# Optimization experiments

Measured on AMD Instinct MI355X. Metric: run time of the kernel, lower is better.

Reference implementation:

```python
import jax, jax.numpy as jnp
import numpy as np

B, T, C = 4, 2048, 384
NUM_HEADS, HEAD_SIZE = 6, 64


def setup_inputs() -> dict:
    key = jax.random.key(0)
    ks = jax.random.split(key, 6)
    s = 1.0 / np.sqrt(C)
    return {
        "x": jax.random.normal(ks[0], (B, T, C), dtype=jnp.float32),
        "Wq": jax.random.normal(ks[1], (C, NUM_HEADS * HEAD_SIZE), dtype=jnp.float32) * s,
        "bq": jnp.zeros((NUM_HEADS * HEAD_SIZE,), dtype=jnp.float32),
        "Wk": jax.random.normal(ks[2], (C, NUM_HEADS * HEAD_SIZE), dtype=jnp.float32) * s,
        "bk": jnp.zeros((NUM_HEADS * HEAD_SIZE,), dtype=jnp.float32),
        "Wv": jax.random.normal(ks[3], (C, NUM_HEADS * HEAD_SIZE), dtype=jnp.float32) * s,
        "bv": jnp.zeros((NUM_HEADS * HEAD_SIZE,), dtype=jnp.float32),
        "Wo": jax.random.normal(ks[4], (NUM_HEADS * HEAD_SIZE, C), dtype=jnp.float32) * s,
        "bo": jnp.zeros((C,), dtype=jnp.float32),
    }


def reference(x, Wq, bq, Wk, bk, Wv, bv, Wo, bo):
    b, t, c = x.shape
    h, d = NUM_HEADS, HEAD_SIZE
    q = (x @ Wq + bq).reshape(b, t, h, d)
    k = (x @ Wk + bk).reshape(b, t, h, d)
    v = (x @ Wv + bv).reshape(b, t, h, d)
    scores = jnp.einsum('bthd,bshd->bhts', q, k) / jnp.sqrt(jnp.float32(d))
    causal = jnp.tril(jnp.ones((t, t), dtype=bool))  # [t,t]
    scores = jnp.where(causal, scores, -jnp.inf)
    weights = jax.nn.softmax(scores, axis=-1)  # dropout identity (inference)
    ctx = jnp.einsum('bhts,bshd->bthd', weights, v).reshape(b, t, h * d)
    return ctx @ Wo + bo
```

## Files before the change

### kernel.cpp

```cpp
#include <hip/hip_runtime.h>

#define B_  4
#define T_  2048
#define C_  384
#define NH_ 6
#define HS_ 64
#define M_  (B_*T_)

typedef float floatx4 __attribute__((ext_vector_type(4)));
typedef __bf16 bf16x8 __attribute__((ext_vector_type(8)));
typedef unsigned short ushort_t;
typedef unsigned short ushortx8 __attribute__((ext_vector_type(8)));
typedef unsigned short ushortx4 __attribute__((ext_vector_type(4)));

__device__ __forceinline__ ushort_t f2bf(float f) {
    unsigned u = __builtin_bit_cast(unsigned, f);
    unsigned r = (u + 0x7FFFu + ((u >> 16) & 1u)) >> 16;
    return (ushort_t)r;
}

__global__ __launch_bounds__(256) void prep(
    const float* __restrict__ x, ushort_t* __restrict__ xb,
    const float* __restrict__ Wq, const float* __restrict__ Wk,
    const float* __restrict__ Wv, const float* __restrict__ Wo,
    ushort_t* __restrict__ Wtq, ushort_t* __restrict__ Wtk,
    ushort_t* __restrict__ Wtv, ushort_t* __restrict__ Wto)
{
    __shared__ float Ls[64][65];
    const int tid = threadIdx.x;
    const int bx = blockIdx.x;

    if (bx < 1536) {
        const int i = (bx * 256 + tid) * 8;
        const float4 a = *(const float4*)&x[i];
        const float4 b = *(const float4*)&x[i + 4];
        ushortx8 p;
        p[0] = f2bf(a.x); p[1] = f2bf(a.y); p[2] = f2bf(a.z); p[3] = f2bf(a.w);
        p[4] = f2bf(b.x); p[5] = f2bf(b.y); p[6] = f2bf(b.z); p[7] = f2bf(b.w);
        *(ushortx8*)&xb[i] = p;
        return;
    }

    const int idx = bx - 1536;
    const int z = idx / 36, rest = idx % 36;
    const float* __restrict__ W = (z == 0) ? Wq : (z == 1) ? Wk : (z == 2) ? Wv : Wo;
    ushort_t* __restrict__ Wt   = (z == 0) ? Wtq : (z == 1) ? Wtk : (z == 2) ? Wtv : Wto;
    const int k0 = (rest / 6) * 64, n0 = (rest % 6) * 64;

    #pragma unroll
    for (int p = 0; p < 4; ++p) {
        const int kk = p * 16 + (tid >> 4);
        const int nn = (tid & 15) * 4;
        const float4 v = *(const float4*)&W[(size_t)(k0 + kk) * 384 + n0 + nn];
        Ls[kk][nn] = v.x; Ls[kk][nn + 1] = v.y; Ls[kk][nn + 2] = v.z; Ls[kk][nn + 3] = v.w;
    }
    __syncthreads();
    #pragma unroll
    for (int p = 0; p < 4; ++p) {
        const int n = p * 16 + (tid >> 4);
        const int kc = (tid & 15) * 4;
        ushortx4 pk;
        #pragma unroll
        for (int t = 0; t < 4; ++t) pk[t] = f2bf(Ls[kc + t][n]);
        *(ushortx4*)&Wt[(size_t)(n0 + n) * 384 + k0 + kc] = pk;
    }
}

__global__ __launch_bounds__(256) void qkv_gemm(
    const ushort_t* __restrict__ xb,
    const ushort_t* __restrict__ Wtq, const ushort_t* __restrict__ Wtk,
    const ushort_t* __restrict__ Wtv,
    const float* __restrict__ bq, const float* __restrict__ bk, const float* __restrict__ bv,
    ushort_t* __restrict__ Qb, ushort_t* __restrict__ Kb, ushort_t* __restrict__ Vtb)
{
    __shared__ ushort_t Sm[2][8192];

    const int tid  = threadIdx.x;
    const int lane = tid & 63;
    const int wv   = tid >> 6;
    const int m    = lane & 15;
    const int quad = lane >> 4;

    const int t0 = blockIdx.x * 128;
    const int n0 = blockIdx.y * 128;
    const int which = n0 / 384;
    const int n_in0 = n0 % 384;
    const bool isV = (which == 2);

    const ushort_t* __restrict__ Wt = (which == 0) ? Wtq : (which == 1) ? Wtk : Wtv;

    const int aOff = isV ? 0 : 4096;
    const int bOff = isV ? 4096 : 0;
    const int a0 = (wv & 1) * 64;
    const int b0 = (wv >> 1) * 64;

    const int rs0 = tid >> 2,         cs0 = tid & 3;
    const int rs1 = (tid + 256) >> 2, cs1 = tid & 3;
    const int sw0 = ((cs0 ^ ((rs0 >> 1) & 3)) << 3);
    const int sw1 = ((cs1 ^ ((rs1 >> 1) & 3)) << 3);

    floatx4 acc[4][4];
    #pragma unroll
    for (int i = 0; i < 4; ++i)
        #pragma unroll
        for (int j = 0; j < 4; ++j) acc[i][j] = (floatx4){0.f, 0.f, 0.f, 0.f};

    ushortx8 xr0 = *(const ushortx8*)&xb[(size_t)(t0 + rs0) * 384 + cs0 * 8];
    ushortx8 xr1 = *(const ushortx8*)&xb[(size_t)(t0 + rs1) * 384 + cs1 * 8];
    ushortx8 wr0 = *(const ushortx8*)&Wt[(size_t)(n_in0 + rs0) * 384 + cs0 * 8];
    ushortx8 wr1 = *(const ushortx8*)&Wt[(size_t)(n_in0 + rs1) * 384 + cs1 * 8];

    for (int ks = 0; ks < 12; ++ks) {
        ushort_t* __restrict__ S = &Sm[ks & 1][0];
        *(ushortx8*)&S[rs0 * 32 + sw0] = xr0;
        *(ushortx8*)&S[rs1 * 32 + sw1] = xr1;
        *(ushortx8*)&S[4096 + rs0 * 32 + sw0] = wr0;
        *(ushortx8*)&S[4096 + rs1 * 32 + sw1] = wr1;
        __syncthreads();

        if (ks < 11) {
            const int kk = (ks + 1) * 32;
            xr0 = *(const ushortx8*)&xb[(size_t)(t0 + rs0) * 384 + kk + cs0 * 8];
            xr1 = *(const ushortx8*)&xb[(size_t)(t0 + rs1) * 384 + kk + cs1 * 8];
            wr0 = *(const ushortx8*)&Wt[(size_t)(n_in0 + rs0) * 384 + kk + cs0 * 8];
            wr1 = *(const ushortx8*)&Wt[(size_t)(n_in0 + rs1) * 384 + kk + cs1 * 8];
        }

        bf16x8 fA[4], fB[4];
        #pragma unroll
        for (int i = 0; i < 4; ++i) {
            const int ra = a0 + i * 16 + m;
            fA[i] = *(const bf16x8*)&S[aOff + ra * 32 + ((quad ^ ((ra >> 1) & 3)) << 3)];
        }
        #pragma unroll
        for (int j = 0; j < 4; ++j) {
            const int rb = b0 + j * 16 + m;
            fB[j] = *(const bf16x8*)&S[bOff + rb * 32 + ((quad ^ ((rb >> 1) & 3)) << 3)];
        }
        #pragma unroll
        for (int i = 0; i < 4; ++i)
            #pragma unroll
            for (int j = 0; j < 4; ++j)
                acc[i][j] = __builtin_amdgcn_mfma_f32_16x16x32_bf16(fA[i], fB[j], acc[i][j], 0, 0, 0);
    }

    if (!isV) {
        ushort_t* __restrict__ out = (which == 0) ? Qb : Kb;
        const float* __restrict__ bias = (which == 0) ? bq : bk;
        const float scale = (which == 0) ? 0.125f : 1.0f;
        #pragma unroll
        for (int i = 0; i < 4; ++i) {
            const int n_base = n_in0 + a0 + i * 16 + quad * 4;
            const int h = n_base >> 6, d0 = n_base & 63;
            #pragma unroll
            for (int j = 0; j < 4; ++j) {
                const int tg = t0 + b0 + j * 16 + m;
                const int b = tg >> 11, tb = tg & (T_ - 1);
                ushortx4 pk;
                #pragma unroll
                for (int r = 0; r < 4; ++r)
                    pk[r] = f2bf((acc[i][j][r] + bias[n_base + r]) * scale);
                *(ushortx4*)&out[(((size_t)(b * NH_ + h)) * T_ + tb) * HS_ + d0] = pk;
            }
        }
    } else {
        #pragma unroll
        for (int i = 0; i < 4; ++i) {
            const int tg0 = t0 + a0 + i * 16 + quad * 4;
            const int b = tg0 >> 11, tb0 = tg0 & (T_ - 1);
            #pragma unroll
            for (int j = 0; j < 4; ++j) {
                const int n_l = n_in0 + b0 + j * 16 + m;
                const int h = n_l >> 6, d = n_l & 63;
                const float bb = bv[n_l];
                ushortx4 pk;
                #pragma unroll
                for (int r = 0; r < 4; ++r) pk[r] = f2bf(acc[i][j][r] + bb);
                *(ushortx4*)&Vtb[(((size_t)(b * NH_ + h)) * HS_ + d) * T_ + tb0] = pk;
            }
        }
    }
}

__global__ __launch_bounds__(256) void proj_gemm(
    const ushort_t* __restrict__ ctxb,
    const ushort_t* __restrict__ Wto,
    const float* __restrict__ bo,
    float* __restrict__ out)
{
    __shared__ ushort_t Sm[2][6144];

    const int tid  = threadIdx.x;
    const int lane = tid & 63;
    const int wv   = tid >> 6;
    const int m    = lane & 15;
    const int quad = lane >> 4;

    const int t0 = blockIdx.x * 64;
    const int n0 = blockIdx.y * 128;
    const int a0 = (wv & 1) * 64;
    const int b0 = (wv >> 1) * 32;

    const int rc = tid >> 2,          cc = tid & 3;
    const int rw0 = tid >> 2,         cw0 = tid & 3;
    const int rw1 = (tid + 256) >> 2, cw1 = tid & 3;
    const int swc  = ((cc  ^ ((rc  >> 1) & 3)) << 3);
    const int sww0 = ((cw0 ^ ((rw0 >> 1) & 3)) << 3);
    const int sww1 = ((cw1 ^ ((rw1 >> 1) & 3)) << 3);

    floatx4 acc[4][2];
    #pragma unroll
    for (int i = 0; i < 4; ++i)
        #pragma unroll
        for (int j = 0; j < 2; ++j) acc[i][j] = (floatx4){0.f, 0.f, 0.f, 0.f};

    ushortx8 cr  = *(const ushortx8*)&ctxb[(size_t)(t0 + rc) * 384 + cc * 8];
    ushortx8 wr0 = *(const ushortx8*)&Wto[(size_t)(n0 + rw0) * 384 + cw0 * 8];
    ushortx8 wr1 = *(const ushortx8*)&Wto[(size_t)(n0 + rw1) * 384 + cw1 * 8];

    for (int ks = 0; ks < 12; ++ks) {
        ushort_t* __restrict__ S = &Sm[ks & 1][0];
        *(ushortx8*)&S[rc * 32 + swc] = cr;
        *(ushortx8*)&S[2048 + rw0 * 32 + sww0] = wr0;
        *(ushortx8*)&S[2048 + rw1 * 32 + sww1] = wr1;
        __syncthreads();

        if (ks < 11) {
            const int kk = (ks + 1) * 32;
            cr  = *(const ushortx8*)&ctxb[(size_t)(t0 + rc) * 384 + kk + cc * 8];
            wr0 = *(const ushortx8*)&Wto[(size_t)(n0 + rw0) * 384 + kk + cw0 * 8];
            wr1 = *(const ushortx8*)&Wto[(size_t)(n0 + rw1) * 384 + kk + cw1 * 8];
        }

        bf16x8 fA[4], fB[2];
        #pragma unroll
        for (int i = 0; i < 4; ++i) {
            const int ra = a0 + i * 16 + m;
            fA[i] = *(const bf16x8*)&S[2048 + ra * 32 + ((quad ^ ((ra >> 1) & 3)) << 3)];
        }
        #pragma unroll
        for (int j = 0; j < 2; ++j) {
            const int rb = b0 + j * 16 + m;
            fB[j] = *(const bf16x8*)&S[rb * 32 + ((quad ^ ((rb >> 1) & 3)) << 3)];
        }
        #pragma unroll
        for (int i = 0; i < 4; ++i)
            #pragma unroll
            for (int j = 0; j < 2; ++j)
                acc[i][j] = __builtin_amdgcn_mfma_f32_16x16x32_bf16(fA[i], fB[j], acc[i][j], 0, 0, 0);
    }

    #pragma unroll
    for (int i = 0; i < 4; ++i) {
        const int n_base = n0 + a0 + i * 16 + quad * 4;
        const float4 bb = *(const float4*)&bo[n_base];
        #pragma unroll
        for (int j = 0; j < 2; ++j) {
            const int tg = t0 + b0 + j * 16 + m;
            float4 o;
            o.x = acc[i][j][0] + bb.x;
            o.y = acc[i][j][1] + bb.y;
            o.z = acc[i][j][2] + bb.z;
            o.w = acc[i][j][3] + bb.w;
            *(float4*)&out[(size_t)tg * 384 + n_base] = o;
        }
    }
}

__global__ __launch_bounds__(256) void attn_mfma(
    const ushort_t* __restrict__ Q,
    const ushort_t* __restrict__ K,
    const ushort_t* __restrict__ Vt,
    ushort_t* __restrict__ ctx)
{
    __shared__ ushort_t Ks[2][64 * 64];
    __shared__ ushort_t Vs[2][64 * 64];
    __shared__ ushort_t Ps[4][16 * 64];

    const int tid  = threadIdx.x;
    const int lane = tid & 63;
    const int wv   = tid >> 6;
    const int m    = lane & 15;
    const int quad = lane >> 4;
    const int cA   = (quad ^ (m & 7)) << 3;

    const int p = blockIdx.x;
    const int h = blockIdx.y, b = blockIdx.z;
    const int bh = b * NH_ + h;

    const int tileHi = 63 - p;
    const int rowbase = ((wv < 2) ? tileHi : p) * 32 + (wv & 1) * 16;
    const int myext = rowbase >> 6;
    const int blockext = tileHi >> 1;

    const ushort_t* __restrict__ Kg = K  + (size_t)bh * (T_ * HS_);
    const ushort_t* __restrict__ Vg = Vt + (size_t)bh * (HS_ * T_);

    const int r0 = tid >> 3,         c0 = tid & 7;
    const int r1 = (tid + 256) >> 3, c1 = tid & 7;
    const int sw0 = ((c0 ^ (r0 & 7)) << 3);
    const int sw1 = ((c1 ^ (r1 & 7)) << 3);

    bf16x8 qf0, qf1;
    {
        const ushort_t* qp = Q + ((size_t)bh * T_ + rowbase + m) * HS_;
        qf0 = *(const bf16x8*)(qp + quad * 8);
        qf1 = *(const bf16x8*)(qp + 32 + quad * 8);
    }

    floatx4 acc_o[4];
    #pragma unroll
    for (int dt = 0; dt < 4; ++dt) acc_o[dt] = (floatx4){0.f, 0.f, 0.f, 0.f};
    float l_lane[4] = {0.f, 0.f, 0.f, 0.f};

    ushort_t* __restrict__ Pw = &Ps[wv][0];

    ushortx8 kr0 = *(const ushortx8*)&Kg[(size_t)r0 * HS_ + c0 * 8];
    ushortx8 kr1 = *(const ushortx8*)&Kg[(size_t)r1 * HS_ + c1 * 8];
    ushortx8 vr0 = *(const ushortx8*)&Vg[(size_t)r0 * T_ + c0 * 8];
    ushortx8 vr1 = *(const ushortx8*)&Vg[(size_t)r1 * T_ + c1 * 8];

    for (int kt = 0; kt <= blockext; ++kt) {
        ushort_t* __restrict__ Kc = &Ks[kt & 1][0];
        ushort_t* __restrict__ Vc = &Vs[kt & 1][0];
        *(ushortx8*)&Kc[r0 * 64 + sw0] = kr0;
        *(ushortx8*)&Kc[r1 * 64 + sw1] = kr1;
        *(ushortx8*)&Vc[r0 * 64 + sw0] = vr0;
        *(ushortx8*)&Vc[r1 * 64 + sw1] = vr1;
        __syncthreads();

        if (kt < blockext) {
            const int s1 = (kt + 1) * 64;
            kr0 = *(const ushortx8*)&Kg[(size_t)(s1 + r0) * HS_ + c0 * 8];
            kr1 = *(const ushortx8*)&Kg[(size_t)(s1 + r1) * HS_ + c1 * 8];
            vr0 = *(const ushortx8*)&Vg[(size_t)r0 * T_ + s1 + c0 * 8];
            vr1 = *(const ushortx8*)&Vg[(size_t)r1 * T_ + s1 + c1 * 8];
        }

        if (kt > myext) continue;

        floatx4 s[4];
        #pragma unroll
        for (int kc = 0; kc < 4; ++kc) {
            const int kb = (kc * 16 + m) * 64;
            bf16x8 k0 = *(const bf16x8*)&Kc[kb + cA];
            bf16x8 k1 = *(const bf16x8*)&Kc[kb + (cA ^ 32)];
            floatx4 a = (floatx4){0.f, 0.f, 0.f, 0.f};
            a = __builtin_amdgcn_mfma_f32_16x16x32_bf16(qf0, k0, a, 0, 0, 0);
            a = __builtin_amdgcn_mfma_f32_16x16x32_bf16(qf1, k1, a, 0, 0, 0);
            s[kc] = a;
        }

        if (kt == myext) {
            #pragma unroll
            for (int kc = 0; kc < 4; ++kc) {
                const int key = kt * 64 + kc * 16 + m;
                #pragma unroll
                for (int r = 0; r < 4; ++r)
                    if (key > rowbase + quad * 4 + r) s[kc][r] = -1e30f;
            }
        }

        const int mc = m >> 3, mp = m & 7;
        #pragma unroll
        for (int r = 0; r < 4; ++r) {
            const int prow = quad * 4 + r;
            const int psw = prow & 7;
            const float p0 = __expf(s[0][r]);
            const float p1 = __expf(s[1][r]);
            const float p2 = __expf(s[2][r]);
            const float p3 = __expf(s[3][r]);
            l_lane[r] += (p0 + p1) + (p2 + p3);
            const int pb = prow * 64 + mp;
            Pw[pb + (((0 + mc) ^ psw) << 3)] = f2bf(p0);
            Pw[pb + (((2 + mc) ^ psw) << 3)] = f2bf(p1);
            Pw[pb + (((4 + mc) ^ psw) << 3)] = f2bf(p2);
            Pw[pb + (((6 + mc) ^ psw) << 3)] = f2bf(p3);
        }
        asm volatile("s_waitcnt lgkmcnt(0)" ::: "memory");
        bf16x8 pf0 = *(const bf16x8*)&Pw[m * 64 + cA];
        bf16x8 pf1 = *(const bf16x8*)&Pw[m * 64 + (cA ^ 32)];

        #pragma unroll
        for (int dt = 0; dt < 4; ++dt) {
            const int vb = (dt * 16 + m) * 64;
            bf16x8 v0 = *(const bf16x8*)&Vc[vb + cA];
            bf16x8 v1 = *(const bf16x8*)&Vc[vb + (cA ^ 32)];
            acc_o[dt] = __builtin_amdgcn_mfma_f32_16x16x32_bf16(pf0, v0, acc_o[dt], 0, 0, 0);
            acc_o[dt] = __builtin_amdgcn_mfma_f32_16x16x32_bf16(pf1, v1, acc_o[dt], 0, 0, 0);
        }
    }

    float l[4];
    #pragma unroll
    for (int r = 0; r < 4; ++r) {
        float ls = l_lane[r];
        ls += __shfl_xor(ls, 1, 64);
        ls += __shfl_xor(ls, 2, 64);
        ls += __shfl_xor(ls, 4, 64);
        ls += __shfl_xor(ls, 8, 64);
        l[r] = ls;
    }
    #pragma unroll
    for (int dt = 0; dt < 4; ++dt) {
        #pragma unroll
        for (int r = 0; r < 4; ++r) {
            const int t = rowbase + quad * 4 + r;
            ctx[((size_t)(b * T_) + t) * C_ + h * HS_ + dt * 16 + m] =
                f2bf(acc_o[dt][r] / l[r]);
        }
    }
}

extern "C" void kernel_launch(void* const* d_in, const int* in_sizes, int n_in,
                              void* d_out, int out_size, void* d_ws, size_t ws_size,
                              hipStream_t stream) {
    const float* x  = (const float*)d_in[0];
    const float* Wq = (const float*)d_in[1];
    const float* bq = (const float*)d_in[2];
    const float* Wk = (const float*)d_in[3];
    const float* bk = (const float*)d_in[4];
    const float* Wv = (const float*)d_in[5];
    const float* bv = (const float*)d_in[6];
    const float* Wo = (const float*)d_in[7];
    const float* bo = (const float*)d_in[8];
    float* out = (float*)d_out;

    const size_t per = (size_t)B_ * NH_ * T_ * HS_;
    const size_t wsz = 384 * 384;
    ushort_t* xb  = (ushort_t*)d_ws;
    ushort_t* Wtq = xb + per;
    ushort_t* Wtk = Wtq + wsz;
    ushort_t* Wtv = Wtk + wsz;
    ushort_t* Wto = Wtv + wsz;
    ushort_t* Qb  = Wto + wsz;
    ushort_t* Kb  = Qb + per;
    ushort_t* Vtb = Kb + per;
    ushort_t* ctxb = Vtb + per;

    prep<<<dim3(1536 + 144), 256, 0, stream>>>(
        x, xb, Wq, Wk, Wv, Wo, Wtq, Wtk, Wtv, Wto);

    qkv_gemm<<<dim3(M_ / 128, 1152 / 128), 256, 0, stream>>>(
        xb, Wtq, Wtk, Wtv, bq, bk, bv, Qb, Kb, Vtb);

    attn_mfma<<<dim3(32, NH_, B_), 256, 0, stream>>>(Qb, Kb, Vtb, ctxb);

    proj_gemm<<<dim3(M_ / 64, 384 / 128), 256, 0, stream>>>(ctxb, Wto, bo, out);
}
```

Measured before the change: 150.5 us.

## Shrink GEMM tiles, remap attention blocks to 64-row tiles with serpentine ordering, truncate P to bf16

The QKV GEMM tile drops from 128x128 to 64x128 and the output projection tile from 64x128 to 64x64, doubling or more the block counts so more CUs are busy. The attention kernel switches from paired high/low 32-row tiles to one 64-row query tile per block. Blocks are ordered longest-first with a serpentine interleave across batch-head to balance the causal work. The bf16 conversion of softmax probabilities now truncates instead of rounding, which saves ALU ops at a small accuracy cost. Smaller tiles reduce per-block data reuse and add more global loads.

Result: faster. 143.5 us (-4.6%).

```diff
diff --git a/kernel.cpp b/kernel.cpp
--- a/kernel.cpp
+++ b/kernel.cpp
@@ -17,6 +17,9 @@
     unsigned u = __builtin_bit_cast(unsigned, f);
     unsigned r = (u + 0x7FFFu + ((u >> 16) & 1u)) >> 16;
     return (ushort_t)r;
+}
+__device__ __forceinline__ ushort_t f2bf_t(float f) {
+    return (ushort_t)(__builtin_bit_cast(unsigned, f) >> 16);
 }
 
 __global__ __launch_bounds__(256) void prep(
@@ -73,7 +76,7 @@
     const float* __restrict__ bq, const float* __restrict__ bk, const float* __restrict__ bv,
     ushort_t* __restrict__ Qb, ushort_t* __restrict__ Kb, ushort_t* __restrict__ Vtb)
 {
-    __shared__ ushort_t Sm[2][8192];
+    __shared__ ushort_t Sm[2][6144];
 
     const int tid  = threadIdx.x;
     const int lane = tid & 63;
@@ -81,7 +84,7 @@
     const int m    = lane & 15;
     const int quad = lane >> 4;
 
-    const int t0 = blockIdx.x * 128;
+    const int t0 = blockIdx.x * 64;
     const int n0 = blockIdx.y * 128;
     const int which = n0 / 384;
     const int n_in0 = n0 % 384;
@@ -89,59 +92,60 @@
 
     const ushort_t* __restrict__ Wt = (which == 0) ? Wtq : (which == 1) ? Wtk : Wtv;
 
-    const int aOff = isV ? 0 : 4096;
-    const int bOff = isV ? 4096 : 0;
-    const int a0 = (wv & 1) * 64;
-    const int b0 = (wv >> 1) * 64;
-
-    const int rs0 = tid >> 2,         cs0 = tid & 3;
-    const int rs1 = (tid + 256) >> 2, cs1 = tid & 3;
-    const int sw0 = ((cs0 ^ ((rs0 >> 1) & 3)) << 3);
-    const int sw1 = ((cs1 ^ ((rs1 >> 1) & 3)) << 3);
-
-    floatx4 acc[4][4];
-    #pragma unroll
-    for (int i = 0; i < 4; ++i)
-        #pragma unroll
-        for (int j = 0; j < 4; ++j) acc[i][j] = (floatx4){0.f, 0.f, 0.f, 0.f};
-
-    ushortx8 xr0 = *(const ushortx8*)&xb[(size_t)(t0 + rs0) * 384 + cs0 * 8];
-    ushortx8 xr1 = *(const ushortx8*)&xb[(size_t)(t0 + rs1) * 384 + cs1 * 8];
-    ushortx8 wr0 = *(const ushortx8*)&Wt[(size_t)(n_in0 + rs0) * 384 + cs0 * 8];
-    ushortx8 wr1 = *(const ushortx8*)&Wt[(size_t)(n_in0 + rs1) * 384 + cs1 * 8];
+    const int tg0 = (wv & 1) * 32;
+    const int ng0 = (wv >> 1) * 64;
+
+    const int rX = tid >> 2, cX = tid & 3;
+    const int swX = ((cX ^ ((rX >> 1) & 3)) << 3);
+    const int rW0 = tid >> 2, rW1 = rW0 + 64, cW = tid & 3;
+    const int swW = ((cW ^ ((rW0 >> 1) & 3)) << 3);
+
+    floatx4 acc[8];
+    #pragma unroll
+    for (int i = 0; i < 8; ++i) acc[i] = (floatx4){0.f, 0.f, 0.f, 0.f};
+
+    ushortx8 xr  = *(const ushortx8*)&xb[(size_t)(t0 + rX) * 384 + cX * 8];
+    ushortx8 wr0 = *(const ushortx8*)&Wt[(size_t)(n_in0 + rW0) * 384 + cW * 8];
+    ushortx8 wr1 = *(const ushortx8*)&Wt[(size_t)(n_in0 + rW1) * 384 + cW * 8];
 
     for (int ks = 0; ks < 12; ++ks) {
         ushort_t* __restrict__ S = &Sm[ks & 1][0];
-        *(ushortx8*)&S[rs0 * 32 + sw0] = xr0;
-        *(ushortx8*)&S[rs1 * 32 + sw1] = xr1;
-        *(ushortx8*)&S[4096 + rs0 * 32 + sw0] = wr0;
-        *(ushortx8*)&S[4096 + rs1 * 32 + sw1] = wr1;
+        *(ushortx8*)&S[rX * 32 + swX] = xr;
+        *(ushortx8*)&S[2048 + rW0 * 32 + swW] = wr0;
+        *(ushortx8*)&S[2048 + rW1 * 32 + swW] = wr1;
         __syncthreads();
 
         if (ks < 11) {
             const int kk = (ks + 1) * 32;
-            xr0 = *(const ushortx8*)&xb[(size_t)(t0 + rs0) * 384 + kk + cs0 * 8];
-            xr1 = *(const ushortx8*)&xb[(size_t)(t0 + rs1) * 384 + kk + cs1 * 8];
-            wr0 = *(const ushortx8*)&Wt[(size_t)(n_in0 + rs0) * 384 + kk + cs0 * 8];
-            wr1 = *(const ushortx8*)&Wt[(size_t)(n_in0 + rs1) * 384 + kk + cs1 * 8];
-        }
-
-        bf16x8 fA[4], fB[4];
+            xr  = *(const ushortx8*)&xb[(size_t)(t0 + rX) * 384 + kk + cX * 8];
+            wr0 = *(const ushortx8*)&Wt[(size_t)(n_in0 + rW0) * 384 + kk + cW * 8];
+            wr1 = *(const ushortx8*)&Wt[(size_t)(n_in0 + rW1) * 384 + kk + cW * 8];
+        }
+
+        bf16x8 fX[2], fW[4];
+        #pragma unroll
+        for (int i = 0; i < 2; ++i) {
+            const int r = tg0 + i * 16 + m;
+            fX[i] = *(const bf16x8*)&S[r * 32 + ((quad ^ ((r >> 1) & 3)) << 3)];
+        }
         #pragma unroll
         for (int i = 0; i < 4; ++i) {
-            const int ra = a0 + i * 16 + m;
-            fA[i] = *(const bf16x8*)&S[aOff + ra * 32 + ((quad ^ ((ra >> 1) & 3)) << 3)];
-        }
-        #pragma unroll
-        for (int j = 0; j < 4; ++j) {
-            const int rb = b0 + j * 16 + m;
-            fB[j] = *(const bf16x8*)&S[bOff + rb * 32 + ((quad ^ ((rb >> 1) & 3)) << 3)];
-        }
-        #pragma unroll
-        for (int i = 0; i < 4; ++i)
-            #pragma unroll
-            for (int j = 0; j < 4; ++j)
-                acc[i][j] = __builtin_amdgcn_mfma_f32_16x16x32_bf16(fA[i], fB[j], acc[i][j], 0, 0, 0);
+            const int r = ng0 + i * 16 + m;
+            fW[i] = *(const bf16x8*)&S[2048 + r * 32 + ((quad ^ ((r >> 1) & 3)) << 3)];
+        }
+        if (isV) {
+            #pragma unroll
+            for (int i = 0; i < 2; ++i)
+                #pragma unroll
+                for (int j = 0; j < 4; ++j)
+                    acc[i * 4 + j] = __builtin_amdgcn_mfma_f32_16x16x32_bf16(fX[i], fW[j], acc[i * 4 + j], 0, 0, 0);
+        } else {
+            #pragma unroll
+            for (int i = 0; i < 4; ++i)
+                #pragma unroll
+                for (int j = 0; j < 2; ++j)
+                    acc[i * 2 + j] = __builtin_amdgcn_mfma_f32_16x16x32_bf16(fW[i], fX[j], acc[i * 2 + j], 0, 0, 0);
+        }
     }
 
     if (!isV) {
@@ -150,32 +154,32 @@
         const float scale = (which == 0) ? 0.125f : 1.0f;
         #pragma unroll
         for (int i = 0; i < 4; ++i) {
-            const int n_base = n_in0 + a0 + i * 16 + quad * 4;
+            const int n_base = n_in0 + ng0 + i * 16 + quad * 4;
             const int h = n_base >> 6, d0 = n_base & 63;
             #pragma unroll
-            for (int j = 0; j < 4; ++j) {
-                const int tg = t0 + b0 + j * 16 + m;
+            for (int j = 0; j < 2; ++j) {
+                const int tg = t0 + tg0 + j * 16 + m;
                 const int b = tg >> 11, tb = tg & (T_ - 1);
                 ushortx4 pk;
                 #pragma unroll
                 for (int r = 0; r < 4; ++r)
-                    pk[r] = f2bf((acc[i][j][r] + bias[n_base + r]) * scale);
+                    pk[r] = f2bf((acc[i * 2 + j][r] + bias[n_base + r]) * scale);
                 *(ushortx4*)&out[(((size_t)(b * NH_ + h)) * T_ + tb) * HS_ + d0] = pk;
             }
         }
     } else {
         #pragma unroll
-        for (int i = 0; i < 4; ++i) {
-            const int tg0 = t0 + a0 + i * 16 + quad * 4;
-            const int b = tg0 >> 11, tb0 = tg0 & (T_ - 1);
+        for (int i = 0; i < 2; ++i) {
+            const int tgq = t0 + tg0 + i * 16 + quad * 4;
+            const int b = tgq >> 11, tb0 = tgq & (T_ - 1);
             #pragma unroll
             for (int j = 0; j < 4; ++j) {
-                const int n_l = n_in0 + b0 + j * 16 + m;
+                const int n_l = n_in0 + ng0 + j * 16 + m;
                 const int h = n_l >> 6, d = n_l & 63;
                 const float bb = bv[n_l];
                 ushortx4 pk;
                 #pragma unroll
-                for (int r = 0; r < 4; ++r) pk[r] = f2bf(acc[i][j][r] + bb);
+                for (int r = 0; r < 4; ++r) pk[r] = f2bf(acc[i * 4 + j][r] + bb);
                 *(ushortx4*)&Vtb[(((size_t)(b * NH_ + h)) * HS_ + d) * T_ + tb0] = pk;
             }
         }
@@ -188,7 +192,7 @@
     const float* __restrict__ bo,
     float* __restrict__ out)
 {
-    __shared__ ushort_t Sm[2][6144];
+    __shared__ ushort_t Sm[2][4096];
 
     const int tid  = threadIdx.x;
     const int lane = tid & 63;
@@ -197,66 +201,56 @@
     const int quad = lane >> 4;
 
     const int t0 = blockIdx.x * 64;
-    const int n0 = blockIdx.y * 128;
-    const int a0 = (wv & 1) * 64;
-    const int b0 = (wv >> 1) * 32;
-
-    const int rc = tid >> 2,          cc = tid & 3;
-    const int rw0 = tid >> 2,         cw0 = tid & 3;
-    const int rw1 = (tid + 256) >> 2, cw1 = tid & 3;
-    const int swc  = ((cc  ^ ((rc  >> 1) & 3)) << 3);
-    const int sww0 = ((cw0 ^ ((rw0 >> 1) & 3)) << 3);
-    const int sww1 = ((cw1 ^ ((rw1 >> 1) & 3)) << 3);
-
-    floatx4 acc[4][2];
-    #pragma unroll
-    for (int i = 0; i < 4; ++i)
+    const int n0 = blockIdx.y * 64;
+    const int tg0 = (wv & 1) * 32;
+    const int ng0 = (wv >> 1) * 32;
+
+    const int rC = tid >> 2, cC = tid & 3;
+    const int swC = ((cC ^ ((rC >> 1) & 3)) << 3);
+
+    floatx4 acc[2][2];
+    #pragma unroll
+    for (int i = 0; i < 2; ++i)
         #pragma unroll
         for (int j = 0; j < 2; ++j) acc[i][j] = (floatx4){0.f, 0.f, 0.f, 0.f};
 
-    ushortx8 cr  = *(const ushortx8*)&ctxb[(size_t)(t0 + rc) * 384 + cc * 8];
-    ushortx8 wr0 = *(const ushortx8*)&Wto[(size_t)(n0 + rw0) * 384 + cw0 * 8];
-    ushortx8 wr1 = *(const ushortx8*)&Wto[(size_t)(n0 + rw1) * 384 + cw1 * 8];
+    ushortx8 cr = *(const ushortx8*)&ctxb[(size_t)(t0 + rC) * 384 + cC * 8];
+    ushortx8 wr = *(const ushortx8*)&Wto[(size_t)(n0 + rC) * 384 + cC * 8];
 
     for (int ks = 0; ks < 12; ++ks) {
         ushort_t* __restrict__ S = &Sm[ks & 1][0];
-        *(ushortx8*)&S[rc * 32 + swc] = cr;
-        *(ushortx8*)&S[2048 + rw0 * 32 + sww0] = wr0;
-        *(ushortx8*)&S[2048 + rw1 * 32 + sww1] = wr1;
+        *(ushortx8*)&S[rC * 32 + swC] = cr;
+        *(ushortx8*)&S[2048 + rC * 32 + swC] = wr;
         __syncthreads();
 
         if (ks < 11) {
             const int kk = (ks + 1) * 32;
-            cr  = *(const ushortx8*)&ctxb[(size_t)(t0 + rc) * 384 + kk + cc * 8];
-            wr0 = *(const ushortx8*)&Wto[(size_t)(n0 + rw0) * 384 + kk + cw0 * 8];
-            wr1 = *(const ushortx8*)&Wto[(size_t)(n0 + rw1) * 384 + kk + cw1 * 8];
-        }
-
-        bf16x8 fA[4], fB[2];
-        #pragma unroll
-        for (int i = 0; i < 4; ++i) {
-            const int ra = a0 + i * 16 + m;
-            fA[i] = *(const bf16x8*)&S[2048 + ra * 32 + ((quad ^ ((ra >> 1) & 3)) << 3)];
-        }
-        #pragma unroll
-        for (int j = 0; j < 2; ++j) {
-            const int rb = b0 + j * 16 + m;
-            fB[j] = *(const bf16x8*)&S[rb * 32 + ((quad ^ ((rb >> 1) & 3)) << 3)];
-        }
-        #pragma unroll
-        for (int i = 0; i < 4; ++i)
+            cr = *(const ushortx8*)&ctxb[(size_t)(t0 + rC) * 384 + kk + cC * 8];
+            wr = *(const ushortx8*)&Wto[(size_t)(n0 + rC) * 384 + kk + cC * 8];
+        }
+
+        bf16x8 fA[2], fB[2];
+        #pragma unroll
+        for (int i = 0; i < 2; ++i) {
+            const int rn = ng0 + i * 16 + m;
+            fA[i] = *(const bf16x8*)&S[2048 + rn * 32 + ((quad ^ ((rn >> 1) & 3)) << 3)];
+            const int rt = tg0 + i * 16 + m;
+            fB[i] = *(const bf16x8*)&S[rt * 32 + ((quad ^ ((rt >> 1) & 3)) << 3)];
+        }
+        #pragma unroll
+        for (int i = 0; i < 2; ++i)
             #pragma unroll
             for (int j = 0; j < 2; ++j)
                 acc[i][j] = __builtin_amdgcn_mfma_f32_16x16x32_bf16(fA[i], fB[j], acc[i][j], 0, 0, 0);
     }
 
     #pragma unroll
-    for (int i = 0; i < 4; ++i) {
-        const int n_base = n0 + a0 + i * 16 + quad * 4;
+    for (int i = 0; i < 2; ++i) {
+        const int n_base = n0 + ng0 + i * 16 + quad * 4;
         const float4 bb = *(const float4*)&bo[n_base];
         #pragma unroll
         for (int j = 0; j < 2; ++j) {
-            const int tg = t0 + b0 + j * 16 + m;
+            const int tg = t0 + tg0 + j * 16 + m;
             float4 o;
             o.x = acc[i][j][0] + bb.x;
             o.y = acc[i][j][1] + bb.y;
@@ -284,14 +278,16 @@
     const int quad = lane >> 4;
     const int cA   = (quad ^ (m & 7)) << 3;
 
-    const int p = blockIdx.x;
-    const int h = blockIdx.y, b = blockIdx.z;
-    const int bh = b * NH_ + h;
-
-    const int tileHi = 63 - p;
-    const int rowbase = ((wv < 2) ? tileHi : p) * 32 + (wv & 1) * 16;
-    const int myext = rowbase >> 6;
-    const int blockext = tileHi >> 1;
+    const int flat = blockIdx.x + 32 * (blockIdx.y + 6 * blockIdx.z);
+    const int rr = flat >> 8, ss = flat & 255;
+    const int rank = (rr << 8) + ((rr & 1) ? (255 - ss) : ss);
+    const int j   = 31 - (rank / 24);
+    const int idx = rank % 24;
+    const int bh  = idx;
+    const int b   = idx / 6, h = idx % 6;
+
+    const int rowbase = j * 64 + wv * 16;
+    const int ext = j;
 
     const ushort_t* __restrict__ Kg = K  + (size_t)bh * (T_ * HS_);
     const ushort_t* __restrict__ Vg = Vt + (size_t)bh * (HS_ * T_);
@@ -320,7 +316,7 @@
     ushortx8 vr0 = *(const ushortx8*)&Vg[(size_t)r0 * T_ + c0 * 8];
     ushortx8 vr1 = *(const ushortx8*)&Vg[(size_t)r1 * T_ + c1 * 8];
 
-    for (int kt = 0; kt <= blockext; ++kt) {
+    for (int kt = 0; kt <= ext; ++kt) {
         ushort_t* __restrict__ Kc = &Ks[kt & 1][0];
         ushort_t* __restrict__ Vc = &Vs[kt & 1][0];
         *(ushortx8*)&Kc[r0 * 64 + sw0] = kr0;
@@ -329,15 +325,13 @@
         *(ushortx8*)&Vc[r1 * 64 + sw1] = vr1;
         __syncthreads();
 
-        if (kt < blockext) {
+        if (kt < ext) {
             const int s1 = (kt + 1) * 64;
             kr0 = *(const ushortx8*)&Kg[(size_t)(s1 + r0) * HS_ + c0 * 8];
             kr1 = *(const ushortx8*)&Kg[(size_t)(s1 + r1) * HS_ + c1 * 8];
             vr0 = *(const ushortx8*)&Vg[(size_t)r0 * T_ + s1 + c0 * 8];
             vr1 = *(const ushortx8*)&Vg[(size_t)r1 * T_ + s1 + c1 * 8];
         }
-
-        if (kt > myext) continue;
 
         floatx4 s[4];
         #pragma unroll
@@ -351,7 +345,7 @@
             s[kc] = a;
         }
 
-        if (kt == myext) {
+        if (kt == ext) {
             #pragma unroll
             for (int kc = 0; kc < 4; ++kc) {
                 const int key = kt * 64 + kc * 16 + m;
@@ -372,10 +366,10 @@
             const float p3 = __expf(s[3][r]);
             l_lane[r] += (p0 + p1) + (p2 + p3);
             const int pb = prow * 64 + mp;
-            Pw[pb + (((0 + mc) ^ psw) << 3)] = f2bf(p0);
-            Pw[pb + (((2 + mc) ^ psw) << 3)] = f2bf(p1);
-            Pw[pb + (((4 + mc) ^ psw) << 3)] = f2bf(p2);
-            Pw[pb + (((6 + mc) ^ psw) << 3)] = f2bf(p3);
+            Pw[pb + (((0 + mc) ^ psw) << 3)] = f2bf_t(p0);
+            Pw[pb + (((2 + mc) ^ psw) << 3)] = f2bf_t(p1);
+            Pw[pb + (((4 + mc) ^ psw) << 3)] = f2bf_t(p2);
+            Pw[pb + (((6 + mc) ^ psw) << 3)] = f2bf_t(p3);
         }
         asm volatile("s_waitcnt lgkmcnt(0)" ::: "memory");
         bf16x8 pf0 = *(const bf16x8*)&Pw[m * 64 + cA];
@@ -441,10 +435,10 @@
     prep<<<dim3(1536 + 144), 256, 0, stream>>>(
         x, xb, Wq, Wk, Wv, Wo, Wtq, Wtk, Wtv, Wto);
 
-    qkv_gemm<<<dim3(M_ / 128, 1152 / 128), 256, 0, stream>>>(
+    qkv_gemm<<<dim3(M_ / 64, 1152 / 128), 256, 0, stream>>>(
         xb, Wtq, Wtk, Wtv, bq, bk, bv, Qb, Kb, Vtb);
 
     attn_mfma<<<dim3(32, NH_, B_), 256, 0, stream>>>(Qb, Kb, Vtb, ctxb);
 
-    proj_gemm<<<dim3(M_ / 64, 384 / 128), 256, 0, stream>>>(ctxb, Wto, bo, out);
-}
+    proj_gemm<<<dim3(M_ / 64, 384 / 64), 256, 0, stream>>>(ctxb, Wto, bo, out);
+}
```
